# Optimization experiments

Hardware: AMD Instinct MI355X
Metric: run time of the kernel (lower is better)

## Reference

```python
import jax, jax.numpy as jnp
import numpy as np

N = 1_000_000   # pose-graph nodes
E = 2_000_000   # edges (odometry + loop closures)
M = N - 1
L1, L2, L3, L4 = 1.0, 0.1, 1.0, 0.1  # loss weights
EPS = 1e-8

# ---- quaternion / Lie-group helpers (pypose convention: [x,y,z,w]) ----

def qmul(q, r):
    qv, qw = q[..., :3], q[..., 3:]
    rv, rw = r[..., :3], r[..., 3:]
    w = qw * rw - jnp.sum(qv * rv, axis=-1, keepdims=True)
    v = qw * rv + rw * qv + jnp.cross(qv, rv)
    return jnp.concatenate([v, w], axis=-1)

def qconj(q):  # inverse of a unit quaternion
    return jnp.concatenate([-q[..., :3], q[..., 3:]], axis=-1)

def qrot(q, v):  # rotate vector v by unit quaternion q
    qv, qw = q[..., :3], q[..., 3:]
    t = 2.0 * jnp.cross(qv, v)
    return v + qw * t + jnp.cross(qv, t)

def so3_log(q):  # SO3 -> so3 rotation vector phi
    v, w = q[..., :3], q[..., 3]
    n = jnp.linalg.norm(v, axis=-1)
    theta = 2.0 * jnp.arctan2(n, w)
    big = n > EPS
    k = jnp.where(big, theta / jnp.where(big, n, 1.0), 2.0 / jnp.where(jnp.abs(w) > EPS, w, 1.0))
    return v * k[..., None]

def se3_log(t, q):  # SE3 -> se3 = [tau(3), phi(3)] (translation first, pypose order)
    phi = so3_log(q)
    theta2 = jnp.sum(phi * phi, axis=-1)
    theta = jnp.sqrt(theta2)
    small = theta < 1e-4
    ts = jnp.where(small, 1.0, theta)
    # V^{-1} coefficient: 1/theta^2 - (1+cos)/(2 theta sin); Taylor -> 1/12
    coef = jnp.where(small, 1.0 / 12.0,
                     1.0 / jnp.where(small, 1.0, theta2)
                     - (1.0 + jnp.cos(ts)) / (2.0 * ts * jnp.sin(ts)))
    pxt = jnp.cross(phi, t)
    tau = t - 0.5 * pxt + coef[..., None] * jnp.cross(phi, pxt)  # V^{-1} t without 3x3 mats
    return jnp.concatenate([tau, phi], axis=-1)

def _unit_quat(key, n):
    q = jax.random.normal(key, (n, 4), dtype=jnp.float32)
    return q / jnp.linalg.norm(q, axis=-1, keepdims=True)

def setup_inputs() -> dict:
    key = jax.random.key(0)
    k = jax.random.split(key, 9)
    nodes = jnp.concatenate([jax.random.normal(k[0], (N, 3), jnp.float32), _unit_quat(k[1], N)], axis=-1)
    vels = jax.random.normal(k[2], (N, 3), jnp.float32)
    edges = jax.random.randint(k[3], (E, 2), 0, N, dtype=jnp.int32)
    poses = jnp.concatenate([jax.random.normal(k[4], (E, 3), jnp.float32), _unit_quat(k[5], E)], axis=-1)
    imu_drots = _unit_quat(k[6], M)
    imu_dtrans = 0.1 * jax.random.normal(k[7], (M, 3), jnp.float32)
    imu_dvels = 0.1 * jax.random.normal(k[8], (M, 3), jnp.float32)
    dts = jnp.full((M, 1), 0.05, dtype=jnp.float32)
    return dict(edges=edges, nodes=nodes, vels=vels, poses=poses,
                imu_drots=imu_drots, imu_dtrans=imu_dtrans, imu_dvels=imu_dvels, dts=dts)

def reference(edges, nodes, vels, poses, imu_drots, imu_dtrans, imu_dvels, dts):
    t_n, q_n = nodes[:, :3], nodes[:, 3:]
    # --- pose-graph residual: (poses^-1 o node1^-1 o node2).Log() ---
    n1 = nodes[edges[:, 0]]
    n2 = nodes[edges[:, 1]]
    t1, q1 = n1[:, :3], n1[:, 3:]
    t2, q2 = n2[:, :3], n2[:, 3:]
    tp, qp = poses[:, :3], poses[:, 3:]
    qi1 = qconj(q1)
    ti1 = -qrot(qi1, t1)           # node1^-1
    qa = qmul(qi1, q2)
    ta = ti1 + qrot(qi1, t2)       # node1^-1 o node2
    qip = qconj(qp)
    tip = -qrot(qip, tp)           # poses^-1
    qe = qmul(qip, qa)
    te = tip + qrot(qip, ta)
    pgerr = se3_log(te, qe)                                   # [E, 6]
    # --- adjacent velocity residual ---
    adjvelerr = imu_dvels - (vels[1:] - vels[:-1])            # [M, 3]
    # --- IMU rotation residual: (drot^-1 o R1^-1 o R2).Log() ---
    qre = qmul(qconj(imu_drots), qmul(qconj(q_n[:-1]), q_n[1:]))
    imuroterr = so3_log(qre)                                  # [M, 3]
    # --- translation/velocity residual ---
    transvelerr = (t_n[1:] - t_n[:-1]) - (vels[:-1] * dts + imu_dtrans)  # [M, 3]
    return jnp.concatenate([L1 * pgerr.ravel(), L2 * adjvelerr.ravel(),
                            L3 * imuroterr.ravel(), L4 * transvelerr.ravel()], axis=0)
```

## Files before the change

kernel.cpp:

```cpp
#include <hip/hip_runtime.h>
#include <hip/hip_fp16.h>
#include <math.h>

#define EPS_Q 1e-8f

struct F3 { float x, y, z; };
struct Q4 { F3 v; float w; };

typedef float    fvec4 __attribute__((ext_vector_type(4)));
typedef unsigned uvec4 __attribute__((ext_vector_type(4)));
typedef int      ivec2 __attribute__((ext_vector_type(2)));

__device__ __forceinline__ F3 add3(F3 a, F3 b){ return {a.x+b.x, a.y+b.y, a.z+b.z}; }
__device__ __forceinline__ F3 sub3(F3 a, F3 b){ return {a.x-b.x, a.y-b.y, a.z-b.z}; }
__device__ __forceinline__ F3 scal3(float s, F3 a){ return {s*a.x, s*a.y, s*a.z}; }
__device__ __forceinline__ float dot3(F3 a, F3 b){ return a.x*b.x + a.y*b.y + a.z*b.z; }
__device__ __forceinline__ F3 cross3(F3 a, F3 b){
    return { a.y*b.z - a.z*b.y, a.z*b.x - a.x*b.z, a.x*b.y - a.y*b.x };
}

__device__ __forceinline__ Q4 qmul(Q4 q, Q4 r){
    Q4 o;
    o.w = q.w*r.w - dot3(q.v, r.v);
    o.v = add3(add3(scal3(q.w, r.v), scal3(r.w, q.v)), cross3(q.v, r.v));
    return o;
}
__device__ __forceinline__ Q4 qconj(Q4 q){ return { {-q.v.x, -q.v.y, -q.v.z}, q.w }; }
__device__ __forceinline__ F3 qrot(Q4 q, F3 v){
    F3 t = scal3(2.0f, cross3(q.v, v));
    return add3(add3(v, scal3(q.w, t)), cross3(q.v, t));
}
__device__ __forceinline__ F3 so3_log(Q4 q){
    float n = sqrtf(dot3(q.v, q.v));
    float theta = 2.0f * atan2f(n, q.w);
    float k;
    if (n > EPS_Q) k = theta / n;
    else           k = 2.0f / ((fabsf(q.w) > EPS_Q) ? q.w : 1.0f);
    return scal3(k, q.v);
}

__device__ __forceinline__ float ntl (const float* p){ return __builtin_nontemporal_load(p); }
__device__ __forceinline__ void  nts (float* p, float v){ __builtin_nontemporal_store(v, p); }

__device__ __forceinline__ unsigned pack2h(float a, float b){
    __half2 h = __floats2half2_rn(a, b);
    unsigned u; __builtin_memcpy(&u, &h, 4);
    return u;
}
__device__ __forceinline__ float2 unp2h(unsigned u){
    __half2 h; __builtin_memcpy(&h, &u, 4);
    return __half22float2(h);
}

template<bool PACK>
__global__ __launch_bounds__(256)
void prep_kernel(const float* __restrict__ nodes,
                 const float* __restrict__ vels,
                 const float* __restrict__ imu_drots,
                 const float* __restrict__ imu_dtrans,
                 const float* __restrict__ imu_dvels,
                 const float* __restrict__ dts,
                 float*       __restrict__ out,
                 uvec4*       __restrict__ nodes16,
                 int N, int M,
                 size_t off_adjvel, size_t off_imurot, size_t off_transvel)
{
    const int m = blockIdx.x * 256 + threadIdx.x;
    if (m >= N) return;

    const float* n0 = nodes + 7*(size_t)m;
    F3 t0 = {n0[0], n0[1], n0[2]};  Q4 q0 = {{n0[3], n0[4], n0[5]}, n0[6]};

    if (PACK) {
        uvec4 row = { pack2h(t0.x, t0.y), pack2h(t0.z, 0.0f),
                      pack2h(q0.v.x, q0.v.y), pack2h(q0.v.z, q0.w) };
        nodes16[m] = row;
    }

    if (m >= M) return;

    const float* n1p = nodes + 7*(size_t)(m+1);
    F3 t1 = {n1p[0], n1p[1], n1p[2]};  Q4 q1 = {{n1p[3], n1p[4], n1p[5]}, n1p[6]};

    F3 v0 = {vels[3*(size_t)m],     vels[3*(size_t)m + 1], vels[3*(size_t)m + 2]};
    F3 v1 = {vels[3*(size_t)m + 3], vels[3*(size_t)m + 4], vels[3*(size_t)m + 5]};

    fvec4 drq = __builtin_nontemporal_load(reinterpret_cast<const fvec4*>(imu_drots) + m);
    Q4 dr = {{drq.x, drq.y, drq.z}, drq.w};

    F3 dvm = { ntl(imu_dvels + 3*(size_t)m),
               ntl(imu_dvels + 3*(size_t)m + 1),
               ntl(imu_dvels + 3*(size_t)m + 2) };
    F3 dtr = { ntl(imu_dtrans + 3*(size_t)m),
               ntl(imu_dtrans + 3*(size_t)m + 1),
               ntl(imu_dtrans + 3*(size_t)m + 2) };
    float dt = ntl(dts + m);

    F3 adjv = sub3(dvm, sub3(v1, v0));
    nts(out + off_adjvel + 3*(size_t)m,     0.1f * adjv.x);
    nts(out + off_adjvel + 3*(size_t)m + 1, 0.1f * adjv.y);
    nts(out + off_adjvel + 3*(size_t)m + 2, 0.1f * adjv.z);

    Q4 qre = qmul(qconj(dr), qmul(qconj(q0), q1));
    F3 rot = so3_log(qre);
    nts(out + off_imurot + 3*(size_t)m,     rot.x);
    nts(out + off_imurot + 3*(size_t)m + 1, rot.y);
    nts(out + off_imurot + 3*(size_t)m + 2, rot.z);

    F3 tv = sub3(sub3(t1, t0), add3(scal3(dt, v0), dtr));
    nts(out + off_transvel + 3*(size_t)m,     0.1f * tv.x);
    nts(out + off_transvel + 3*(size_t)m + 1, 0.1f * tv.y);
    nts(out + off_transvel + 3*(size_t)m + 2, 0.1f * tv.z);
}

__device__ __forceinline__ void edge_body(F3 t1, Q4 q1, F3 t2, Q4 q2,
                                          const float* __restrict__ p,
                                          float* __restrict__ o)
{
    F3 tp = {ntl(p+0), ntl(p+1), ntl(p+2)};
    Q4 qp = {{ntl(p+3), ntl(p+4), ntl(p+5)}, ntl(p+6)};

    Q4 qi1 = qconj(q1);
    F3 ti1 = scal3(-1.0f, qrot(qi1, t1));
    Q4 qa  = qmul(qi1, q2);
    F3 ta  = add3(ti1, qrot(qi1, t2));

    Q4 qip = qconj(qp);
    F3 tip = scal3(-1.0f, qrot(qip, tp));
    Q4 qe  = qmul(qip, qa);
    F3 te  = add3(tip, qrot(qip, ta));

    F3 phi = so3_log(qe);
    float theta2 = dot3(phi, phi);
    float theta  = sqrtf(theta2);
    float coef;
    if (theta < 1e-4f) {
        coef = 1.0f / 12.0f;
    } else {
        float s, c;
        sincosf(theta, &s, &c);
        coef = 1.0f / theta2 - (1.0f + c) / (2.0f * theta * s);
    }
    F3 pxt = cross3(phi, te);
    F3 tau = add3(sub3(te, scal3(0.5f, pxt)), scal3(coef, cross3(phi, pxt)));

    nts(o,   tau.x); nts(o+1, tau.y); nts(o+2, tau.z);
    nts(o+3, phi.x); nts(o+4, phi.y); nts(o+5, phi.z);
}

__global__ __launch_bounds__(256)
void edge_kernel_packed(const int*   __restrict__ edges,
                        const uvec4* __restrict__ nodes16,
                        const float* __restrict__ poses,
                        float*       __restrict__ out,
                        int E)
{
    const int e = blockIdx.x * 256 + threadIdx.x;
    if (e >= E) return;

    ivec2 ij = __builtin_nontemporal_load(reinterpret_cast<const ivec2*>(edges) + e);

    uvec4 r1 = nodes16[ij.x];
    uvec4 r2 = nodes16[ij.y];

    float2 a0 = unp2h(r1.x), a1 = unp2h(r1.y), a2 = unp2h(r1.z), a3 = unp2h(r1.w);
    float2 b0 = unp2h(r2.x), b1 = unp2h(r2.y), b2 = unp2h(r2.z), b3 = unp2h(r2.w);

    F3 t1 = {a0.x, a0.y, a1.x};  Q4 q1 = {{a2.x, a2.y, a3.x}, a3.y};
    F3 t2 = {b0.x, b0.y, b1.x};  Q4 q2 = {{b2.x, b2.y, b3.x}, b3.y};

    edge_body(t1, q1, t2, q2, poses + 7*(size_t)e, out + 6*(size_t)e);
}

__global__ __launch_bounds__(256)
void edge_kernel_direct(const int*   __restrict__ edges,
                        const float* __restrict__ nodes,
                        const float* __restrict__ poses,
                        float*       __restrict__ out,
                        int E)
{
    const int e = blockIdx.x * 256 + threadIdx.x;
    if (e >= E) return;

    ivec2 ij = __builtin_nontemporal_load(reinterpret_cast<const ivec2*>(edges) + e);
    const float* n1 = nodes + 7*(size_t)ij.x;
    const float* n2 = nodes + 7*(size_t)ij.y;

    F3 t1 = {n1[0], n1[1], n1[2]};  Q4 q1 = {{n1[3], n1[4], n1[5]}, n1[6]};
    F3 t2 = {n2[0], n2[1], n2[2]};  Q4 q2 = {{n2[3], n2[4], n2[5]}, n2[6]};

    edge_body(t1, q1, t2, q2, poses + 7*(size_t)e, out + 6*(size_t)e);
}

extern "C" void kernel_launch(void* const* d_in, const int* in_sizes, int n_in,
                              void* d_out, int out_size, void* d_ws, size_t ws_size,
                              hipStream_t stream) {
    const int*   edges      = (const int*)  d_in[0];
    const float* nodes      = (const float*)d_in[1];
    const float* vels       = (const float*)d_in[2];
    const float* poses      = (const float*)d_in[3];
    const float* imu_drots  = (const float*)d_in[4];
    const float* imu_dtrans = (const float*)d_in[5];
    const float* imu_dvels  = (const float*)d_in[6];
    const float* dts        = (const float*)d_in[7];
    float* out = (float*)d_out;

    const int E = in_sizes[0] / 2;
    const int N = in_sizes[1] / 7;
    const int M = in_sizes[7];

    const size_t off_adjvel   = 6*(size_t)E;
    const size_t off_imurot   = off_adjvel + 3*(size_t)M;
    const size_t off_transvel = off_imurot + 3*(size_t)M;

    const int BLK = 256;
    const int NBLKS = (N + BLK - 1) / BLK;
    const int EBLKS = (E + BLK - 1) / BLK;

    uvec4* nodes16 = (uvec4*)d_ws;
    const bool can_pack = (d_ws != nullptr) && (ws_size >= (size_t)N * 16);

    if (can_pack) {
        prep_kernel<true><<<NBLKS, BLK, 0, stream>>>(nodes, vels, imu_drots, imu_dtrans,
                                                     imu_dvels, dts, out, nodes16, N, M,
                                                     off_adjvel, off_imurot, off_transvel);
        edge_kernel_packed<<<EBLKS, BLK, 0, stream>>>(edges, nodes16, poses, out, E);
    } else {
        prep_kernel<false><<<NBLKS, BLK, 0, stream>>>(nodes, vels, imu_drots, imu_dtrans,
                                                      imu_dvels, dts, out, nullptr, N, M,
                                                      off_adjvel, off_imurot, off_transvel);
        edge_kernel_direct<<<EBLKS, BLK, 0, stream>>>(edges, nodes, poses, out, E);
    }
}
```

Before: 263.9 us.

## Split prep into a fast pack kernel and move node residuals after edges

The prep kernel that both packed nodes to fp16 and computed the IMU residuals is split in two. A lightweight pack kernel stages node rows through shared memory for coalesced loads, and the IMU residual kernel now runs after the edge kernel. The edge kernel processes two edges per thread with vectorized index loads, which gives more memory-level parallelism per thread. The aim is to shorten the critical path before the edge kernel and improve load coalescing, at the cost of an extra launch and re-reading the nodes.

```diff
diff --git a/kernel.cpp b/kernel.cpp
--- a/kernel.cpp
+++ b/kernel.cpp
@@ -10,6 +10,7 @@
 typedef float    fvec4 __attribute__((ext_vector_type(4)));
 typedef unsigned uvec4 __attribute__((ext_vector_type(4)));
 typedef int      ivec2 __attribute__((ext_vector_type(2)));
+typedef int      ivec4 __attribute__((ext_vector_type(4)));
 
 __device__ __forceinline__ F3 add3(F3 a, F3 b){ return {a.x+b.x, a.y+b.y, a.z+b.z}; }
 __device__ __forceinline__ F3 sub3(F3 a, F3 b){ return {a.x-b.x, a.y-b.y, a.z-b.z}; }
@@ -52,74 +53,33 @@
     return __half22float2(h);
 }
 
-template<bool PACK>
-__global__ __launch_bounds__(256)
-void prep_kernel(const float* __restrict__ nodes,
-                 const float* __restrict__ vels,
-                 const float* __restrict__ imu_drots,
-                 const float* __restrict__ imu_dtrans,
-                 const float* __restrict__ imu_dvels,
-                 const float* __restrict__ dts,
-                 float*       __restrict__ out,
-                 uvec4*       __restrict__ nodes16,
-                 int N, int M,
-                 size_t off_adjvel, size_t off_imurot, size_t off_transvel)
-{
-    const int m = blockIdx.x * 256 + threadIdx.x;
-    if (m >= N) return;
-
-    const float* n0 = nodes + 7*(size_t)m;
-    F3 t0 = {n0[0], n0[1], n0[2]};  Q4 q0 = {{n0[3], n0[4], n0[5]}, n0[6]};
-
-    if (PACK) {
-        uvec4 row = { pack2h(t0.x, t0.y), pack2h(t0.z, 0.0f),
-                      pack2h(q0.v.x, q0.v.y), pack2h(q0.v.z, q0.w) };
-        nodes16[m] = row;
-    }
-
-    if (m >= M) return;
-
-    const float* n1p = nodes + 7*(size_t)(m+1);
-    F3 t1 = {n1p[0], n1p[1], n1p[2]};  Q4 q1 = {{n1p[3], n1p[4], n1p[5]}, n1p[6]};
-
-    F3 v0 = {vels[3*(size_t)m],     vels[3*(size_t)m + 1], vels[3*(size_t)m + 2]};
-    F3 v1 = {vels[3*(size_t)m + 3], vels[3*(size_t)m + 4], vels[3*(size_t)m + 5]};
-
-    fvec4 drq = __builtin_nontemporal_load(reinterpret_cast<const fvec4*>(imu_drots) + m);
-    Q4 dr = {{drq.x, drq.y, drq.z}, drq.w};
-
-    F3 dvm = { ntl(imu_dvels + 3*(size_t)m),
-               ntl(imu_dvels + 3*(size_t)m + 1),
-               ntl(imu_dvels + 3*(size_t)m + 2) };
-    F3 dtr = { ntl(imu_dtrans + 3*(size_t)m),
-               ntl(imu_dtrans + 3*(size_t)m + 1),
-               ntl(imu_dtrans + 3*(size_t)m + 2) };
-    float dt = ntl(dts + m);
-
-    F3 adjv = sub3(dvm, sub3(v1, v0));
-    nts(out + off_adjvel + 3*(size_t)m,     0.1f * adjv.x);
-    nts(out + off_adjvel + 3*(size_t)m + 1, 0.1f * adjv.y);
-    nts(out + off_adjvel + 3*(size_t)m + 2, 0.1f * adjv.z);
-
-    Q4 qre = qmul(qconj(dr), qmul(qconj(q0), q1));
-    F3 rot = so3_log(qre);
-    nts(out + off_imurot + 3*(size_t)m,     rot.x);
-    nts(out + off_imurot + 3*(size_t)m + 1, rot.y);
-    nts(out + off_imurot + 3*(size_t)m + 2, rot.z);
-
-    F3 tv = sub3(sub3(t1, t0), add3(scal3(dt, v0), dtr));
-    nts(out + off_transvel + 3*(size_t)m,     0.1f * tv.x);
-    nts(out + off_transvel + 3*(size_t)m + 1, 0.1f * tv.y);
-    nts(out + off_transvel + 3*(size_t)m + 2, 0.1f * tv.z);
-}
-
-__device__ __forceinline__ void edge_body(F3 t1, Q4 q1, F3 t2, Q4 q2,
-                                          const float* __restrict__ p,
-                                          float* __restrict__ o)
-{
-    F3 tp = {ntl(p+0), ntl(p+1), ntl(p+2)};
-    Q4 qp = {{ntl(p+3), ntl(p+4), ntl(p+5)}, ntl(p+6)};
-
+__global__ __launch_bounds__(256)
+void pack_kernel(const float* __restrict__ nodes, uvec4* __restrict__ nodes16, int N)
+{
+    __shared__ float s[7*256];
+    const int tid  = threadIdx.x;
+    const int base = blockIdx.x * 256;
+    const int nrows = min(256, N - base);
+    const int ndw   = nrows * 7;
+
+    #pragma unroll
+    for (int k = 0; k < 7; ++k) {
+        int idx = k*256 + tid;
+        if (idx < ndw) s[idx] = ntl(nodes + (size_t)base*7 + idx);
+    }
+    __syncthreads();
+
+    if (tid < nrows) {
+        const float* r = s + 7*tid;
+        uvec4 row = { pack2h(r[0], r[1]), pack2h(r[2], 0.0f),
+                      pack2h(r[3], r[4]), pack2h(r[5], r[6]) };
+        __builtin_nontemporal_store(row, nodes16 + base + tid);
+    }
+}
+
+__device__ __forceinline__ void edge_math(F3 t1, Q4 q1, F3 t2, Q4 q2,
+                                          F3 tp, Q4 qp, float* __restrict__ o)
+{
     Q4 qi1 = qconj(q1);
     F3 ti1 = scal3(-1.0f, qrot(qi1, t1));
     Q4 qa  = qmul(qi1, q2);
@@ -148,28 +108,61 @@
     nts(o+3, phi.x); nts(o+4, phi.y); nts(o+5, phi.z);
 }
 
-__global__ __launch_bounds__(256)
-void edge_kernel_packed(const int*   __restrict__ edges,
-                        const uvec4* __restrict__ nodes16,
-                        const float* __restrict__ poses,
-                        float*       __restrict__ out,
-                        int E)
-{
-    const int e = blockIdx.x * 256 + threadIdx.x;
-    if (e >= E) return;
-
-    ivec2 ij = __builtin_nontemporal_load(reinterpret_cast<const ivec2*>(edges) + e);
-
-    uvec4 r1 = nodes16[ij.x];
-    uvec4 r2 = nodes16[ij.y];
-
+__device__ __forceinline__ void unpack_rows(uvec4 r1, uvec4 r2,
+                                            F3& t1, Q4& q1, F3& t2, Q4& q2)
+{
     float2 a0 = unp2h(r1.x), a1 = unp2h(r1.y), a2 = unp2h(r1.z), a3 = unp2h(r1.w);
     float2 b0 = unp2h(r2.x), b1 = unp2h(r2.y), b2 = unp2h(r2.z), b3 = unp2h(r2.w);
-
-    F3 t1 = {a0.x, a0.y, a1.x};  Q4 q1 = {{a2.x, a2.y, a3.x}, a3.y};
-    F3 t2 = {b0.x, b0.y, b1.x};  Q4 q2 = {{b2.x, b2.y, b3.x}, b3.y};
-
-    edge_body(t1, q1, t2, q2, poses + 7*(size_t)e, out + 6*(size_t)e);
+    t1 = {a0.x, a0.y, a1.x};  q1 = {{a2.x, a2.y, a3.x}, a3.y};
+    t2 = {b0.x, b0.y, b1.x};  q2 = {{b2.x, b2.y, b3.x}, b3.y};
+}
+
+__global__ __launch_bounds__(256)
+void edge_kernel2(const int*   __restrict__ edges,
+                  const uvec4* __restrict__ nodes16,
+                  const float* __restrict__ poses,
+                  float*       __restrict__ out,
+                  int E)
+{
+    const int t  = blockIdx.x * 256 + threadIdx.x;
+    const int e0 = 2*t, e1 = 2*t + 1;
+    if (e0 >= E) return;
+    const bool has1 = (e1 < E);
+
+    ivec4 ij;
+    if (has1) {
+        ij = __builtin_nontemporal_load(reinterpret_cast<const ivec4*>(edges) + t);
+    } else {
+        ivec2 a = __builtin_nontemporal_load(reinterpret_cast<const ivec2*>(edges) + e0);
+        ij = {a.x, a.y, a.x, a.y};
+    }
+
+    uvec4 r1a = nodes16[ij.x];
+    uvec4 r2a = nodes16[ij.y];
+    uvec4 r1b = nodes16[ij.z];
+    uvec4 r2b = nodes16[ij.w];
+
+    const float* p = poses + 7*(size_t)e0;
+    float pv[14];
+    #pragma unroll
+    for (int k = 0; k < 7; ++k) pv[k] = ntl(p + k);
+    if (has1) {
+        #pragma unroll
+        for (int k = 7; k < 14; ++k) pv[k] = ntl(p + k);
+    }
+
+    F3 t1, t2; Q4 q1, q2;
+    unpack_rows(r1a, r2a, t1, q1, t2, q2);
+    edge_math(t1, q1, t2, q2,
+              F3{pv[0], pv[1], pv[2]}, Q4{{pv[3], pv[4], pv[5]}, pv[6]},
+              out + 6*(size_t)e0);
+
+    if (has1) {
+        unpack_rows(r1b, r2b, t1, q1, t2, q2);
+        edge_math(t1, q1, t2, q2,
+                  F3{pv[7], pv[8], pv[9]}, Q4{{pv[10], pv[11], pv[12]}, pv[13]},
+                  out + 6*(size_t)e1);
+    }
 }
 
 __global__ __launch_bounds__(256)
@@ -185,11 +178,63 @@
     ivec2 ij = __builtin_nontemporal_load(reinterpret_cast<const ivec2*>(edges) + e);
     const float* n1 = nodes + 7*(size_t)ij.x;
     const float* n2 = nodes + 7*(size_t)ij.y;
+    const float* p  = poses + 7*(size_t)e;
 
     F3 t1 = {n1[0], n1[1], n1[2]};  Q4 q1 = {{n1[3], n1[4], n1[5]}, n1[6]};
     F3 t2 = {n2[0], n2[1], n2[2]};  Q4 q2 = {{n2[3], n2[4], n2[5]}, n2[6]};
-
-    edge_body(t1, q1, t2, q2, poses + 7*(size_t)e, out + 6*(size_t)e);
+    edge_math(t1, q1, t2, q2,
+              F3{ntl(p+0), ntl(p+1), ntl(p+2)}, Q4{{ntl(p+3), ntl(p+4), ntl(p+5)}, ntl(p+6)},
+              out + 6*(size_t)e);
+}
+
+__global__ __launch_bounds__(256)
+void node_kernel(const float* __restrict__ nodes,
+                 const float* __restrict__ vels,
+                 const float* __restrict__ imu_drots,
+                 const float* __restrict__ imu_dtrans,
+                 const float* __restrict__ imu_dvels,
+                 const float* __restrict__ dts,
+                 float*       __restrict__ out,
+                 int M,
+                 size_t off_adjvel, size_t off_imurot, size_t off_transvel)
+{
+    const int m = blockIdx.x * 256 + threadIdx.x;
+    if (m >= M) return;
+
+    const float* n0 = nodes + 7*(size_t)m;
+    const float* n1 = nodes + 7*(size_t)(m+1);
+    F3 t0 = {n0[0], n0[1], n0[2]};  Q4 q0 = {{n0[3], n0[4], n0[5]}, n0[6]};
+    F3 t1 = {n1[0], n1[1], n1[2]};  Q4 q1 = {{n1[3], n1[4], n1[5]}, n1[6]};
+
+    F3 v0 = {vels[3*(size_t)m],     vels[3*(size_t)m + 1], vels[3*(size_t)m + 2]};
+    F3 v1 = {vels[3*(size_t)m + 3], vels[3*(size_t)m + 4], vels[3*(size_t)m + 5]};
+
+    fvec4 drq = __builtin_nontemporal_load(reinterpret_cast<const fvec4*>(imu_drots) + m);
+    Q4 dr = {{drq.x, drq.y, drq.z}, drq.w};
+
+    F3 dvm = { ntl(imu_dvels + 3*(size_t)m),
+               ntl(imu_dvels + 3*(size_t)m + 1),
+               ntl(imu_dvels + 3*(size_t)m + 2) };
+    F3 dtr = { ntl(imu_dtrans + 3*(size_t)m),
+               ntl(imu_dtrans + 3*(size_t)m + 1),
+               ntl(imu_dtrans + 3*(size_t)m + 2) };
+    float dt = ntl(dts + m);
+
+    F3 adjv = sub3(dvm, sub3(v1, v0));
+    nts(out + off_adjvel + 3*(size_t)m,     0.1f * adjv.x);
+    nts(out + off_adjvel + 3*(size_t)m + 1, 0.1f * adjv.y);
+    nts(out + off_adjvel + 3*(size_t)m + 2, 0.1f * adjv.z);
+
+    Q4 qre = qmul(qconj(dr), qmul(qconj(q0), q1));
+    F3 rot = so3_log(qre);
+    nts(out + off_imurot + 3*(size_t)m,     rot.x);
+    nts(out + off_imurot + 3*(size_t)m + 1, rot.y);
+    nts(out + off_imurot + 3*(size_t)m + 2, rot.z);
+
+    F3 tv = sub3(sub3(t1, t0), add3(scal3(dt, v0), dtr));
+    nts(out + off_transvel + 3*(size_t)m,     0.1f * tv.x);
+    nts(out + off_transvel + 3*(size_t)m + 1, 0.1f * tv.y);
+    nts(out + off_transvel + 3*(size_t)m + 2, 0.1f * tv.z);
 }
 
 extern "C" void kernel_launch(void* const* d_in, const int* in_sizes, int n_in,
@@ -214,21 +259,16 @@
     const size_t off_transvel = off_imurot + 3*(size_t)M;
 
     const int BLK = 256;
-    const int NBLKS = (N + BLK - 1) / BLK;
-    const int EBLKS = (E + BLK - 1) / BLK;
-
     uvec4* nodes16 = (uvec4*)d_ws;
     const bool can_pack = (d_ws != nullptr) && (ws_size >= (size_t)N * 16);
 
     if (can_pack) {
-        prep_kernel<true><<<NBLKS, BLK, 0, stream>>>(nodes, vels, imu_drots, imu_dtrans,
-                                                     imu_dvels, dts, out, nodes16, N, M,
-                                                     off_adjvel, off_imurot, off_transvel);
-        edge_kernel_packed<<<EBLKS, BLK, 0, stream>>>(edges, nodes16, poses, out, E);
+        pack_kernel<<<(N + BLK - 1)/BLK, BLK, 0, stream>>>(nodes, nodes16, N);
+        edge_kernel2<<<(E + 2*BLK - 1)/(2*BLK), BLK, 0, stream>>>(edges, nodes16, poses, out, E);
     } else {
-        prep_kernel<false><<<NBLKS, BLK, 0, stream>>>(nodes, vels, imu_drots, imu_dtrans,
-                                                      imu_dvels, dts, out, nullptr, N, M,
-                                                      off_adjvel, off_imurot, off_transvel);
-        edge_kernel_direct<<<EBLKS, BLK, 0, stream>>>(edges, nodes, poses, out, E);
-    }
-}
+        edge_kernel_direct<<<(E + BLK - 1)/BLK, BLK, 0, stream>>>(edges, nodes, poses, out, E);
+    }
+    node_kernel<<<(M + BLK - 1)/BLK, BLK, 0, stream>>>(nodes, vels, imu_drots, imu_dtrans,
+                                                       imu_dvels, dts, out, M,
+                                                       off_adjvel, off_imurot, off_transvel);
+}
```

Result: slower. 297.1 us (+12.6%).
